# Performance work log

Hardware: AMD Instinct MI355X
Metric: run time of the kernel (lower is better)

Reference implementation:

```python
import jax, jax.numpy as jnp
import numpy as np

AUDIO_DIM, SEM_DIM, ATTN_DIM = 512, 768, 128


def setup_inputs() -> dict:
    key = jax.random.key(0)
    ks = jax.random.split(key, 12)
    B, T, T_sem = 8, 4096, 1024
    s = lambda d: 1.0 / np.sqrt(d)
    return {
        "x_ct": jax.random.normal(ks[0], (B, AUDIO_DIM, T), jnp.float32),
        "sem_btd": jax.random.normal(ks[1], (B, T_sem, SEM_DIM), jnp.float32),
        "ln_w": jnp.ones((AUDIO_DIM,), jnp.float32),
        "ln_b": jnp.zeros((AUDIO_DIM,), jnp.float32),
        "Wq": jax.random.normal(ks[2], (AUDIO_DIM, ATTN_DIM), jnp.float32) * s(AUDIO_DIM),
        "bq": jnp.zeros((ATTN_DIM,), jnp.float32),
        "Wk": jax.random.normal(ks[3], (SEM_DIM, ATTN_DIM), jnp.float32) * s(SEM_DIM),
        "bk": jnp.zeros((ATTN_DIM,), jnp.float32),
        "Wv": jax.random.normal(ks[4], (SEM_DIM, ATTN_DIM), jnp.float32) * s(SEM_DIM),
        "bv": jnp.zeros((ATTN_DIM,), jnp.float32),
        "Wo": jax.random.normal(ks[5], (ATTN_DIM, AUDIO_DIM), jnp.float32) * s(ATTN_DIM),
        "bo": jnp.zeros((AUDIO_DIM,), jnp.float32),
    }


def _layernorm(x, w, b, eps=1e-5):
    mu = jnp.mean(x, axis=-1, keepdims=True)
    var = jnp.mean(jnp.square(x - mu), axis=-1, keepdims=True)
    return (x - mu) * jax.lax.rsqrt(var + eps) * w + b


def reference(x_ct, sem_btd, ln_w, ln_b, Wq, bq, Wk, bk, Wv, bv, Wo, bo):
    # x_ct: [B, C, T] -> [B, T, C]
    x = jnp.swapaxes(x_ct, 1, 2)
    x = _layernorm(x, ln_w, ln_b)
    Q = x @ Wq + bq                      # [B, T, A]
    K = sem_btd @ Wk + bk                # [B, S, A]
    V = sem_btd @ Wv + bv                # [B, S, A]
    scale = ATTN_DIM ** -0.5
    attn = jnp.einsum("bta,bsa->bts", Q, K) * scale
    attn = jax.nn.softmax(attn, axis=-1)  # dropout: eval mode (identity)
    ctx = jnp.einsum("bts,bsa->bta", attn, V)
    delta = ctx @ Wo + bo                # [B, T, C]
    return jnp.swapaxes(delta, 1, 2)     # [B, C, T]
```

## Files before the change

### kernel.cpp

```cpp
#include <hip/hip_runtime.h>
#include <hip/hip_bf16.h>
#include <math.h>

#define BATCH 8
#define TDIM 4096
#define SDIM 1024
#define CDIM 512
#define DDIM 768
#define ADIM 128

typedef short s8v __attribute__((ext_vector_type(8)));
typedef float f4v __attribute__((ext_vector_type(4)));

__device__ __forceinline__ short f2bf(float f) {
    unsigned u = __float_as_uint(f);
    u += 0x7fffu + ((u >> 16) & 1u);
    return (short)(u >> 16);
}
__device__ __forceinline__ float bf2f(short s) {
    return __uint_as_float(((unsigned)(unsigned short)s) << 16);
}
__device__ __forceinline__ f4v mfma16(s8v a, s8v b, f4v c) {
    return __builtin_amdgcn_mfma_f32_16x16x32_bf16(a, b, c, 0, 0, 0);
}
__device__ __forceinline__ void gl_lds16(const short* g, short* l) {
    __builtin_amdgcn_global_load_lds(
        (const __attribute__((address_space(1))) unsigned int*)g,
        (__attribute__((address_space(3))) unsigned int*)l, 16, 0, 0);
}

__global__ __launch_bounds__(256) void prep_w(
    const float* __restrict__ Wq, const float* __restrict__ Wk,
    const float* __restrict__ Wv, const float* __restrict__ Wo,
    const float* __restrict__ lnw,
    short* __restrict__ WqT, short* __restrict__ WkT,
    short* __restrict__ WvT, short* __restrict__ WoT,
    float* __restrict__ uq)
{
    int gid = blockIdx.x * 256 + threadIdx.x;
    if (blockIdx.x == 0) uq[threadIdx.x] = 0.f;
    {
        int k = gid >> 7, n = gid & 127;
        int idx = (k >> 6) * 8192 + n * 64 + ((((k >> 3) & 7) ^ (n & 7)) * 8) + (k & 7);
        WqT[idx] = f2bf(Wq[gid] * lnw[k]);
    }
    #pragma unroll
    for (int i = 0; i < 2; ++i) {
        int e = gid + i * 65536;
        if (e < 98304) {
            int k = e >> 7, n = e & 127;
            WkT[n * 768 + k] = f2bf(Wk[e]);
            WvT[n * 768 + k] = f2bf(Wv[e]);
        }
    }
    {
        int k = gid >> 9, c = gid & 511;
        WoT[c * 128 + k] = f2bf(Wo[gid]);
    }
}

__global__ __launch_bounds__(256) void prep_uv(
    const float* __restrict__ Wq, const float* __restrict__ lnw,
    const float* __restrict__ lnb,
    float* __restrict__ uq, float* __restrict__ vq)
{
    __shared__ float r1[128], r2[128];
    const int a = threadIdx.x & 127, h = threadIdx.x >> 7;
    const int c = blockIdx.x * 2 + h;
    float wv = Wq[c * 128 + a];
    float s1 = bf2f(f2bf(lnw[c] * wv));
    float s2 = lnb[c] * wv;
    if (h) { r1[a] = s1; r2[a] = s2; }
    __syncthreads();
    if (!h) {
        atomicAdd(&uq[a], s1 + r1[a]);
        atomicAdd(&vq[a], s2 + r2[a]);
    }
}

__global__ __launch_bounds__(256) void kv_proj(
    const float* __restrict__ sem,
    const short* __restrict__ WkT, const float* __restrict__ bk,
    const short* __restrict__ WvT, const float* __restrict__ bv,
    short* __restrict__ Kb, short* __restrict__ Vb)
{
    __shared__ __align__(16) short sA[32 * 40];
    __shared__ __align__(16) short sW[2][128 * 40];
    const int tid = threadIdx.x, lane = tid & 63, wave = tid >> 6;
    const int ln15 = lane & 15, q = lane >> 4, kq = q * 8;
    const int r0 = blockIdx.x * 32;
    const int b = r0 >> 10, sbase = r0 & 1023;
    const int kv = wave >> 1;
    const int mh = wave & 1;
    const int m  = mh * 16 + ln15;

    f4v acc[8];
    #pragma unroll
    for (int j = 0; j < 8; ++j) acc[j] = (f4v)0.0f;

    const int srow = tid >> 3;
    const int sk4  = (tid & 7) * 4;

    for (int kc = 0; kc < DDIM / 32; ++kc) {
        __syncthreads();
        {
            float4 f = *(const float4*)&sem[(size_t)(r0 + srow) * DDIM + kc * 32 + sk4];
            uint2 pk;
            pk.x = (unsigned short)f2bf(f.x) | ((unsigned)(unsigned short)f2bf(f.y) << 16);
            pk.y = (unsigned short)f2bf(f.z) | ((unsigned)(unsigned short)f2bf(f.w) << 16);
            *(uint2*)&sA[srow * 40 + sk4] = pk;
        }
        #pragma unroll
        for (int i = 0; i < 2; ++i) {
            int idx8 = i * 256 + tid;
            int n = idx8 >> 2, k8 = (idx8 & 3) * 8;
            *(s8v*)&sW[0][n * 40 + k8] = *(const s8v*)&WkT[(size_t)n * 768 + kc * 32 + k8];
            *(s8v*)&sW[1][n * 40 + k8] = *(const s8v*)&WvT[(size_t)n * 768 + kc * 32 + k8];
        }
        __syncthreads();
        s8v a = *(const s8v*)&sA[m * 40 + kq];
        #pragma unroll
        for (int j = 0; j < 8; ++j) {
            s8v bb = *(const s8v*)&sW[kv][(j * 16 + ln15) * 40 + kq];
            acc[j] = mfma16(a, bb, acc[j]);
        }
    }
    const int s_in_b = sbase + mh * 16 + q * 4;
    if (kv == 0) {
        #pragma unroll
        for (int j = 0; j < 8; ++j) {
            int col = j * 16 + ln15;
            float bias = bk[col];
            #pragma unroll
            for (int r = 0; r < 4; ++r)
                Kb[((size_t)b * SDIM + s_in_b + r) * ADIM + col] = f2bf(acc[j][r] + bias);
        }
    } else {
        #pragma unroll
        for (int j = 0; j < 8; ++j) {
            int col = j * 16 + ln15;
            float bias = bv[col];
            uint2 pk;
            pk.x = (unsigned short)f2bf(acc[j][0] + bias) | ((unsigned)(unsigned short)f2bf(acc[j][1] + bias) << 16);
            pk.y = (unsigned short)f2bf(acc[j][2] + bias) | ((unsigned)(unsigned short)f2bf(acc[j][3] + bias) << 16);
            *(uint2*)&Vb[((size_t)b * ADIM + col) * SDIM + s_in_b] = pk;
        }
    }
}

__global__ __launch_bounds__(512, 4) void ln_q(
    const float* __restrict__ x,
    const short* __restrict__ WqI, const float* __restrict__ uq,
    const float* __restrict__ vq, const float* __restrict__ bq,
    short* __restrict__ Qb)
{
    __shared__ __align__(16) short sX[2][64 * 72];
    __shared__ __align__(16) short sW[2][64 * 128];
    __shared__ __align__(16) float redw[8][16][4][2];
    const int tid = threadIdx.x, lane = tid & 63, wave = tid >> 6;
    const int ln15 = lane & 15, q = lane >> 4, kq = q * 8;
    const int b = blockIdx.x >> 6;
    const int t0 = (blockIdx.x & 63) * 64;
    const float* xb = x + (size_t)b * CDIM * TDIM + t0;

    const int rg = lane >> 4;
    const int g  = rg & 1;
    const int L  = lane & 15;
    const int t4 = L * 4;
    const int crow = wave * 4 + rg;

    float ps1[4] = {0.f,0.f,0.f,0.f}, ps2[4] = {0.f,0.f,0.f,0.f};
    const int wr = wave & 3, wc = wave >> 2;
    const int m = wr * 16 + ln15;
    const int swzm = (m >> 2) & 7;
    f4v acc[4];
    #pragma unroll
    for (int j = 0; j < 4; ++j) acc[j] = (f4v)0.0f;

    float4 xv[2];

#define PROC_X(BUF) do {                                                      \
    _Pragma("unroll")                                                         \
    for (int i = 0; i < 2; ++i) {                                             \
        float4 v = xv[i];                                                     \
        ps1[0] += v.x; ps2[0] += v.x * v.x;                                   \
        ps1[1] += v.y; ps2[1] += v.y * v.y;                                   \
        ps1[2] += v.z; ps2[2] += v.z * v.z;                                   \
        ps1[3] += v.w; ps2[3] += v.w * v.w;                                   \
        float o0 = __shfl_xor(v.x, 16); float o1 = __shfl_xor(v.y, 16);       \
        float o2 = __shfl_xor(v.z, 16); float o3 = __shfl_xor(v.w, 16);       \
        const int c   = crow + i * 32;                                        \
        const int cdw = c & ~1;                                               \
        unsigned wA, wB; int tA, tB;                                          \
        if (g == 0) {                                                         \
            tA = t4; tB = t4 + 1;                                             \
            wA = (unsigned short)f2bf(v.x) | ((unsigned)(unsigned short)f2bf(o0) << 16); \
            wB = (unsigned short)f2bf(v.y) | ((unsigned)(unsigned short)f2bf(o1) << 16); \
        } else {                                                              \
            tA = t4 + 2; tB = t4 + 3;                                         \
            wA = (unsigned short)f2bf(o2) | ((unsigned)(unsigned short)f2bf(v.z) << 16); \
            wB = (unsigned short)f2bf(o3) | ((unsigned)(unsigned short)f2bf(v.w) << 16); \
        }                                                                     \
        *(unsigned*)&sX[BUF][tA * 72 + (((cdw >> 3) ^ ((tA >> 2) & 7)) * 8) + (cdw & 7)] = wA; \
        *(unsigned*)&sX[BUF][tB * 72 + (((cdw >> 3) ^ ((tB >> 2) & 7)) * 8) + (cdw & 7)] = wB; \
    }                                                                         \
} while (0)

    xv[0] = *(const float4*)&xb[(size_t)crow * TDIM + t4];
    xv[1] = *(const float4*)&xb[(size_t)(crow + 32) * TDIM + t4];
    #pragma unroll
    for (int i = 0; i < 2; ++i) {
        int gi = i * 512 + wave * 64;
        gl_lds16(&WqI[(size_t)(gi + lane) * 8], &sW[0][gi * 8]);
    }
    PROC_X(0);
    __syncthreads();

    for (int kc = 0; kc < 8; ++kc) {
        const int cur = kc & 1;
        if (kc < 7) {
            const float* xc = xb + (size_t)(kc + 1) * 64 * TDIM;
            xv[0] = *(const float4*)&xc[(size_t)crow * TDIM + t4];
            xv[1] = *(const float4*)&xc[(size_t)(crow + 32) * TDIM + t4];
            const short* wch = WqI + (size_t)(kc + 1) * 8192;
            #pragma unroll
            for (int i = 0; i < 2; ++i) {
                int gi = i * 512 + wave * 64;
                gl_lds16(&wch[(size_t)(gi + lane) * 8], &sW[cur ^ 1][gi * 8]);
            }
        }
        #pragma unroll
        for (int kk = 0; kk < 2; ++kk) {
            s8v a = *(const s8v*)&sX[cur][m * 72 + (((kk * 4 + q) ^ swzm) * 8)];
            #pragma unroll
            for (int j = 0; j < 4; ++j) {
                int n = wc * 64 + j * 16 + ln15;
                s8v bb = *(const s8v*)&sW[cur][n * 64 + (((kk * 4 + q) ^ (n & 7)) * 8)];
                acc[j] = mfma16(a, bb, acc[j]);
            }
        }
        if (kc < 7) PROC_X(cur ^ 1);
        __syncthreads();
    }

    #pragma unroll
    for (int mk = 16; mk <= 32; mk <<= 1) {
        #pragma unroll
        for (int jj = 0; jj < 4; ++jj) {
            ps1[jj] += __shfl_xor(ps1[jj], mk);
            ps2[jj] += __shfl_xor(ps2[jj], mk);
        }
    }
    if (lane < 16) {
        #pragma unroll
        for (int jj = 0; jj < 4; ++jj) {
            redw[wave][L][jj][0] = ps1[jj];
            redw[wave][L][jj][1] = ps2[jj];
        }
    }
    __syncthreads();

    float u4[4], v4[4];
    #pragma unroll
    for (int j = 0; j < 4; ++j) {
        int col = wc * 64 + j * 16 + ln15;
        u4[j] = uq[col]; v4[j] = vq[col] + bq[col];
    }
    const float scale = 0.08838834764831845f;
    const int quad = wr * 4 + q;
    #pragma unroll
    for (int r = 0; r < 4; ++r) {
        float s1 = 0.f, s2 = 0.f;
        #pragma unroll
        for (int w = 0; w < 8; ++w) {
            float2 p = *(const float2*)&redw[w][quad][r][0];
            s1 += p.x; s2 += p.y;
        }
        float mu = s1 * (1.f / 512.f);
        float var = s2 * (1.f / 512.f) - mu * mu;
        float rs = rsqrtf(var + 1e-5f);
        int t = t0 + wr * 16 + q * 4 + r;
        #pragma unroll
        for (int j = 0; j < 4; ++j) {
            float qv = (rs * (acc[j][r] - mu * u4[j]) + v4[j]) * scale;
            Qb[((size_t)b * TDIM + t) * ADIM + (wc * 64 + j * 16 + ln15)] = f2bf(qv);
        }
    }
#undef PROC_X
}

__global__ __launch_bounds__(256) void attn(
    const short* __restrict__ Qb, const short* __restrict__ Kb,
    const short* __restrict__ Vb, short* __restrict__ Cx)
{
    __shared__ __align__(16) short sK [2][64 * 128];
    __shared__ __align__(16) short sVT[2][128 * 64];
    __shared__ __align__(16) short sP [64 * 64];
    const int tid = threadIdx.x, lane = tid & 63, wave = tid >> 6;
    const int ln15 = lane & 15, q = lane >> 4, kq = q * 8;
    const int b = blockIdx.x >> 6;
    const int t0 = (blockIdx.x & 63) * 64;
    const int m = wave * 16 + ln15;

    const int krow = tid >> 4, kkb = tid & 15;
    const int varow = tid >> 3, vkb = tid & 7;

    s8v qf[4];
    {
        const short* qp = Qb + ((size_t)b * TDIM + t0 + m) * ADIM + kq;
        #pragma unroll
        for (int kc = 0; kc < 4; ++kc) qf[kc] = *(const s8v*)(qp + kc * 32);
    }
    s8v ones;
    #pragma unroll
    for (int j = 0; j < 8; ++j) ones[j] = (short)0x3F80;

    f4v accO[8]; f4v accL = (f4v)0.0f;
    #pragma unroll
    for (int j = 0; j < 8; ++j) accO[j] = (f4v)0.0f;

    const short* Kbase = Kb + (size_t)b * SDIM * ADIM;
    const short* Vbase = Vb + (size_t)b * ADIM * SDIM;
    s8v rk[4], rv[4];

    #pragma unroll
    for (int i = 0; i < 4; ++i) {
        rk[i] = *(const s8v*)(Kbase + (size_t)(i * 16 + krow) * ADIM + kkb * 8);
        rv[i] = *(const s8v*)(Vbase + (size_t)(i * 32 + varow) * SDIM + vkb * 8);
    }
    #pragma unroll
    for (int i = 0; i < 4; ++i) {
        int r = i * 16 + krow;
        *(s8v*)&sK[0][r * 128 + ((kkb ^ (r & 15)) * 8)] = rk[i];
        int a = i * 32 + varow;
        *(s8v*)&sVT[0][a * 64 + ((vkb ^ (a & 7)) * 8)] = rv[i];
    }
    __syncthreads();

    for (int sc = 0; sc < SDIM / 64; ++sc) {
        const int cur = sc & 1;
        if (sc < 15) {
            const int s0n = (sc + 1) * 64;
            #pragma unroll
            for (int i = 0; i < 4; ++i) {
                rk[i] = *(const s8v*)(Kbase + (size_t)(s0n + i * 16 + krow) * ADIM + kkb * 8);
                rv[i] = *(const s8v*)(Vbase + (size_t)(i * 32 + varow) * SDIM + s0n + vkb * 8);
            }
        }
        #pragma unroll
        for (int j = 0; j < 4; ++j) {
            f4v sacc = (f4v)0.0f;
            const int row = j * 16 + ln15;
            #pragma unroll
            for (int kc = 0; kc < 4; ++kc) {
                s8v bb = *(const s8v*)&sK[cur][row * 128 + (((kc * 4 + q) ^ (row & 15)) * 8)];
                sacc = mfma16(qf[kc], bb, sacc);
            }
            #pragma unroll
            for (int r = 0; r < 4; ++r) {
                float ev = __expf(sacc[r]);
                int prow = wave * 16 + q * 4 + r;
                int pcol = j * 16 + ln15;
                sP[prow * 64 + (((pcol >> 3) ^ (prow & 7)) * 8) + (pcol & 7)] = f2bf(ev);
            }
        }
        #pragma unroll
        for (int kc = 0; kc < 2; ++kc) {
            s8v pa = *(const s8v*)&sP[m * 64 + (((kc * 4 + q) ^ (m & 7)) * 8)];
            accL = mfma16(pa, ones, accL);
            #pragma unroll
            for (int j = 0; j < 8; ++j) {
                int a = j * 16 + ln15;
                s8v bb = *(const s8v*)&sVT[cur][a * 64 + (((kc * 4 + q) ^ (a & 7)) * 8)];
                accO[j] = mfma16(pa, bb, accO[j]);
            }
        }
        if (sc < 15) {
            #pragma unroll
            for (int i = 0; i < 4; ++i) {
                int r = i * 16 + krow;
                *(s8v*)&sK[cur ^ 1][r * 128 + ((kkb ^ (r & 15)) * 8)] = rk[i];
                int a = i * 32 + varow;
                *(s8v*)&sVT[cur ^ 1][a * 64 + ((vkb ^ (a & 7)) * 8)] = rv[i];
            }
        }
        __syncthreads();
    }
    #pragma unroll
    for (int r = 0; r < 4; ++r) {
        float rinv = 1.0f / accL[r];
        int t = t0 + wave * 16 + q * 4 + r;
        #pragma unroll
        for (int j = 0; j < 8; ++j) {
            int col = j * 16 + ln15;
            Cx[((size_t)b * TDIM + t) * ADIM + col] = f2bf(accO[j][r] * rinv);
        }
    }
}

__global__ __launch_bounds__(256) void out_proj(
    const short* __restrict__ Cx, const short* __restrict__ WoT,
    const float* __restrict__ bo, float* __restrict__ out)
{
    __shared__ __align__(16) short sCtx[64 * 136];
    __shared__ __align__(16) char  buf[128 * 136 * 2];
    short* sWoT = (short*)buf;
    float* outT = (float*)buf;
    const int tid = threadIdx.x, lane = tid & 63, wave = tid >> 6;
    const int ln15 = lane & 15, q = lane >> 4, kq = q * 8;
    const int b = blockIdx.x >> 8;
    const int rem = blockIdx.x & 255;
    const int t0 = (rem & 63) * 64;
    const int c0 = (rem >> 6) * 128;

    #pragma unroll
    for (int i = 0; i < 4; ++i) {
        int idx8 = i * 256 + tid;
        int row = idx8 >> 4, a8 = (idx8 & 15) * 8;
        *(s8v*)&sCtx[row * 136 + a8] = *(const s8v*)&Cx[((size_t)b * TDIM + t0 + row) * ADIM + a8];
    }
    #pragma unroll
    for (int i = 0; i < 8; ++i) {
        int idx8 = i * 256 + tid;
        int n = idx8 >> 4, k8 = (idx8 & 15) * 8;
        *(s8v*)&sWoT[n * 136 + k8] = *(const s8v*)&WoT[(size_t)(c0 + n) * ADIM + k8];
    }
    __syncthreads();
    f4v acc[8];
    #pragma unroll
    for (int j = 0; j < 8; ++j) acc[j] = (f4v)0.0f;
    const int m = wave * 16 + ln15;
    #pragma unroll
    for (int kc = 0; kc < 4; ++kc) {
        s8v a = *(const s8v*)&sCtx[m * 136 + kc * 32 + kq];
        #pragma unroll
        for (int j = 0; j < 8; ++j) {
            s8v bb = *(const s8v*)&sWoT[(j * 16 + ln15) * 136 + kc * 32 + kq];
            acc[j] = mfma16(a, bb, acc[j]);
        }
    }
    __syncthreads();
    #pragma unroll
    for (int j = 0; j < 8; ++j) {
        int cl = j * 16 + ln15;
        float bias = bo[c0 + cl];
        #pragma unroll
        for (int r = 0; r < 4; ++r) {
            int tl = wave * 16 + q * 4 + r;
            outT[cl * 68 + tl] = acc[j][r] + bias;
        }
    }
    __syncthreads();
    #pragma unroll
    for (int i = 0; i < 8; ++i) {
        int idx4 = i * 256 + tid;
        int c = idx4 >> 4, t4 = (idx4 & 15) * 4;
        float4 v = *(const float4*)&outT[c * 68 + t4];
        *(float4*)&out[((size_t)b * CDIM + c0 + c) * TDIM + t0 + t4] = v;
    }
}

extern "C" void kernel_launch(void* const* d_in, const int* in_sizes, int n_in,
                              void* d_out, int out_size, void* d_ws, size_t ws_size,
                              hipStream_t stream) {
    const float* x   = (const float*)d_in[0];
    const float* sem = (const float*)d_in[1];
    const float* lnw = (const float*)d_in[2];
    const float* lnb = (const float*)d_in[3];
    const float* Wq  = (const float*)d_in[4];
    const float* bq  = (const float*)d_in[5];
    const float* Wk  = (const float*)d_in[6];
    const float* bk  = (const float*)d_in[7];
    const float* Wv  = (const float*)d_in[8];
    const float* bv  = (const float*)d_in[9];
    const float* Wo  = (const float*)d_in[10];
    const float* bo  = (const float*)d_in[11];
    float* out = (float*)d_out;

    short* ws  = (short*)d_ws;
    short* Qb  = ws;
    short* Kb  = Qb  + (size_t)BATCH * TDIM * ADIM;
    short* Vb  = Kb  + (size_t)BATCH * SDIM * ADIM;
    short* Cx  = Vb  + (size_t)BATCH * SDIM * ADIM;
    short* WqT = Cx  + (size_t)BATCH * TDIM * ADIM;
    short* WkT = WqT + 128 * 512;
    short* WvT = WkT + 128 * 768;
    short* WoT = WvT + 128 * 768;
    float* uq  = (float*)(WoT + 512 * 128);
    float* vq  = uq + 128;

    hipLaunchKernelGGL(prep_w,  dim3(256),  dim3(256), 0, stream,
                       Wq, Wk, Wv, Wo, lnw, WqT, WkT, WvT, WoT, uq);
    hipLaunchKernelGGL(prep_uv, dim3(256),  dim3(256), 0, stream, Wq, lnw, lnb, uq, vq);
    hipLaunchKernelGGL(kv_proj, dim3(256),  dim3(256), 0, stream, sem, WkT, bk, WvT, bv, Kb, Vb);
    hipLaunchKernelGGL(ln_q,    dim3(512),  dim3(512), 0, stream, x, WqT, uq, vq, bq, Qb);
    hipLaunchKernelGGL(attn,    dim3(512),  dim3(256), 0, stream, Qb, Kb, Vb, Cx);
    hipLaunchKernelGGL(out_proj,dim3(2048), dim3(256), 0, stream, Cx, WoT, bo, out);
}
```

Baseline: 234.1 us.

## Merge prep kernels and co-schedule LN-Q with KV projection in one launch

After: 232.9 us. Within noise of the previous version (-0.5%).

```diff
diff --git a/kernel.cpp b/kernel.cpp
--- a/kernel.cpp
+++ b/kernel.cpp
@@ -29,155 +29,88 @@
         (__attribute__((address_space(3))) unsigned int*)l, 16, 0, 0);
 }
 
-__global__ __launch_bounds__(256) void prep_w(
+__global__ __launch_bounds__(256) void prep(
     const float* __restrict__ Wq, const float* __restrict__ Wk,
     const float* __restrict__ Wv, const float* __restrict__ Wo,
-    const float* __restrict__ lnw,
+    const float* __restrict__ lnw, const float* __restrict__ lnb,
     short* __restrict__ WqT, short* __restrict__ WkT,
     short* __restrict__ WvT, short* __restrict__ WoT,
-    float* __restrict__ uq)
-{
-    int gid = blockIdx.x * 256 + threadIdx.x;
-    if (blockIdx.x == 0) uq[threadIdx.x] = 0.f;
-    {
-        int k = gid >> 7, n = gid & 127;
-        int idx = (k >> 6) * 8192 + n * 64 + ((((k >> 3) & 7) ^ (n & 7)) * 8) + (k & 7);
-        WqT[idx] = f2bf(Wq[gid] * lnw[k]);
-    }
-    #pragma unroll
-    for (int i = 0; i < 2; ++i) {
-        int e = gid + i * 65536;
-        if (e < 98304) {
-            int k = e >> 7, n = e & 127;
-            WkT[n * 768 + k] = f2bf(Wk[e]);
-            WvT[n * 768 + k] = f2bf(Wv[e]);
-        }
-    }
-    {
-        int k = gid >> 9, c = gid & 511;
-        WoT[c * 128 + k] = f2bf(Wo[gid]);
-    }
-}
-
-__global__ __launch_bounds__(256) void prep_uv(
-    const float* __restrict__ Wq, const float* __restrict__ lnw,
-    const float* __restrict__ lnb,
     float* __restrict__ uq, float* __restrict__ vq)
 {
     __shared__ float r1[128], r2[128];
-    const int a = threadIdx.x & 127, h = threadIdx.x >> 7;
-    const int c = blockIdx.x * 2 + h;
-    float wv = Wq[c * 128 + a];
-    float s1 = bf2f(f2bf(lnw[c] * wv));
-    float s2 = lnb[c] * wv;
-    if (h) { r1[a] = s1; r2[a] = s2; }
-    __syncthreads();
-    if (!h) {
-        atomicAdd(&uq[a], s1 + r1[a]);
-        atomicAdd(&vq[a], s2 + r2[a]);
-    }
-}
-
-__global__ __launch_bounds__(256) void kv_proj(
+    if (blockIdx.x < 256) {
+        int gid = blockIdx.x * 256 + threadIdx.x;
+        {
+            int k = gid >> 7, n = gid & 127;
+            int idx = (k >> 6) * 8192 + n * 64 + ((((k >> 3) & 7) ^ (n & 7)) * 8) + (k & 7);
+            WqT[idx] = f2bf(Wq[gid] * lnw[k]);
+        }
+        #pragma unroll
+        for (int i = 0; i < 2; ++i) {
+            int e = gid + i * 65536;
+            if (e < 98304) {
+                int k = e >> 7, n = e & 127;
+                WkT[n * 768 + k] = f2bf(Wk[e]);
+                WvT[n * 768 + k] = f2bf(Wv[e]);
+            }
+        }
+        {
+            int k = gid >> 9, c = gid & 511;
+            WoT[c * 128 + k] = f2bf(Wo[gid]);
+        }
+    } else {
+        const int a = threadIdx.x & 127, h = threadIdx.x >> 7;
+        const int c = (blockIdx.x - 256) * 2 + h;
+        float wv = Wq[c * 128 + a];
+        float s1 = bf2f(f2bf(lnw[c] * wv));
+        float s2 = lnb[c] * wv;
+        if (h) { r1[a] = s1; r2[a] = s2; }
+        __syncthreads();
+        if (!h) {
+            atomicAdd(&uq[a], s1 + r1[a]);
+            atomicAdd(&vq[a], s2 + r2[a]);
+        }
+    }
+}
+
+__global__ __launch_bounds__(512, 4) void mid(
+    const float* __restrict__ x, const short* __restrict__ WqI,
+    const float* __restrict__ uq, const float* __restrict__ vq,
+    const float* __restrict__ bq, short* __restrict__ Qb,
     const float* __restrict__ sem,
     const short* __restrict__ WkT, const float* __restrict__ bk,
     const short* __restrict__ WvT, const float* __restrict__ bv,
     short* __restrict__ Kb, short* __restrict__ Vb)
 {
-    __shared__ __align__(16) short sA[32 * 40];
-    __shared__ __align__(16) short sW[2][128 * 40];
+    __shared__ __align__(16) char smem[55296];
     const int tid = threadIdx.x, lane = tid & 63, wave = tid >> 6;
     const int ln15 = lane & 15, q = lane >> 4, kq = q * 8;
-    const int r0 = blockIdx.x * 32;
-    const int b = r0 >> 10, sbase = r0 & 1023;
-    const int kv = wave >> 1;
-    const int mh = wave & 1;
-    const int m  = mh * 16 + ln15;
-
-    f4v acc[8];
-    #pragma unroll
-    for (int j = 0; j < 8; ++j) acc[j] = (f4v)0.0f;
-
-    const int srow = tid >> 3;
-    const int sk4  = (tid & 7) * 4;
-
-    for (int kc = 0; kc < DDIM / 32; ++kc) {
-        __syncthreads();
-        {
-            float4 f = *(const float4*)&sem[(size_t)(r0 + srow) * DDIM + kc * 32 + sk4];
-            uint2 pk;
-            pk.x = (unsigned short)f2bf(f.x) | ((unsigned)(unsigned short)f2bf(f.y) << 16);
-            pk.y = (unsigned short)f2bf(f.z) | ((unsigned)(unsigned short)f2bf(f.w) << 16);
-            *(uint2*)&sA[srow * 40 + sk4] = pk;
-        }
-        #pragma unroll
-        for (int i = 0; i < 2; ++i) {
-            int idx8 = i * 256 + tid;
-            int n = idx8 >> 2, k8 = (idx8 & 3) * 8;
-            *(s8v*)&sW[0][n * 40 + k8] = *(const s8v*)&WkT[(size_t)n * 768 + kc * 32 + k8];
-            *(s8v*)&sW[1][n * 40 + k8] = *(const s8v*)&WvT[(size_t)n * 768 + kc * 32 + k8];
-        }
-        __syncthreads();
-        s8v a = *(const s8v*)&sA[m * 40 + kq];
-        #pragma unroll
-        for (int j = 0; j < 8; ++j) {
-            s8v bb = *(const s8v*)&sW[kv][(j * 16 + ln15) * 40 + kq];
-            acc[j] = mfma16(a, bb, acc[j]);
-        }
-    }
-    const int s_in_b = sbase + mh * 16 + q * 4;
-    if (kv == 0) {
-        #pragma unroll
-        for (int j = 0; j < 8; ++j) {
-            int col = j * 16 + ln15;
-            float bias = bk[col];
-            #pragma unroll
-            for (int r = 0; r < 4; ++r)
-                Kb[((size_t)b * SDIM + s_in_b + r) * ADIM + col] = f2bf(acc[j][r] + bias);
-        }
-    } else {
-        #pragma unroll
-        for (int j = 0; j < 8; ++j) {
-            int col = j * 16 + ln15;
-            float bias = bv[col];
-            uint2 pk;
-            pk.x = (unsigned short)f2bf(acc[j][0] + bias) | ((unsigned)(unsigned short)f2bf(acc[j][1] + bias) << 16);
-            pk.y = (unsigned short)f2bf(acc[j][2] + bias) | ((unsigned)(unsigned short)f2bf(acc[j][3] + bias) << 16);
-            *(uint2*)&Vb[((size_t)b * ADIM + col) * SDIM + s_in_b] = pk;
-        }
-    }
-}
-
-__global__ __launch_bounds__(512, 4) void ln_q(
-    const float* __restrict__ x,
-    const short* __restrict__ WqI, const float* __restrict__ uq,
-    const float* __restrict__ vq, const float* __restrict__ bq,
-    short* __restrict__ Qb)
-{
-    __shared__ __align__(16) short sX[2][64 * 72];
-    __shared__ __align__(16) short sW[2][64 * 128];
-    __shared__ __align__(16) float redw[8][16][4][2];
-    const int tid = threadIdx.x, lane = tid & 63, wave = tid >> 6;
-    const int ln15 = lane & 15, q = lane >> 4, kq = q * 8;
-    const int b = blockIdx.x >> 6;
-    const int t0 = (blockIdx.x & 63) * 64;
-    const float* xb = x + (size_t)b * CDIM * TDIM + t0;
-
-    const int rg = lane >> 4;
-    const int g  = rg & 1;
-    const int L  = lane & 15;
-    const int t4 = L * 4;
-    const int crow = wave * 4 + rg;
-
-    float ps1[4] = {0.f,0.f,0.f,0.f}, ps2[4] = {0.f,0.f,0.f,0.f};
-    const int wr = wave & 3, wc = wave >> 2;
-    const int m = wr * 16 + ln15;
-    const int swzm = (m >> 2) & 7;
-    f4v acc[4];
-    #pragma unroll
-    for (int j = 0; j < 4; ++j) acc[j] = (f4v)0.0f;
-
-    float4 xv[2];
+    const int bid = blockIdx.x;
+
+    if ((bid % 3) != 2) {
+        const int ln_id = (bid / 3) * 2 + (bid % 3);
+        short* sXp = (short*)smem;
+        short* sWp = (short*)(smem + 18432);
+        float* redwp = (float*)(smem + 51200);
+        const int b = ln_id >> 6;
+        const int t0 = (ln_id & 63) * 64;
+        const float* xb = x + (size_t)b * CDIM * TDIM + t0;
+
+        const int rg = lane >> 4;
+        const int g  = rg & 1;
+        const int L  = lane & 15;
+        const int t4 = L * 4;
+        const int crow = wave * 4 + rg;
+
+        float ps1[4] = {0.f,0.f,0.f,0.f}, ps2[4] = {0.f,0.f,0.f,0.f};
+        const int wr = wave & 3, wc = wave >> 2;
+        const int m = wr * 16 + ln15;
+        const int swzm = (m >> 2) & 7;
+        f4v acc[4];
+        #pragma unroll
+        for (int j = 0; j < 4; ++j) acc[j] = (f4v)0.0f;
+
+        float4 xv[2];
 
 #define PROC_X(BUF) do {                                                      \
     _Pragma("unroll")                                                         \
@@ -201,92 +134,159 @@
             wA = (unsigned short)f2bf(o2) | ((unsigned)(unsigned short)f2bf(v.z) << 16); \
             wB = (unsigned short)f2bf(o3) | ((unsigned)(unsigned short)f2bf(v.w) << 16); \
         }                                                                     \
-        *(unsigned*)&sX[BUF][tA * 72 + (((cdw >> 3) ^ ((tA >> 2) & 7)) * 8) + (cdw & 7)] = wA; \
-        *(unsigned*)&sX[BUF][tB * 72 + (((cdw >> 3) ^ ((tB >> 2) & 7)) * 8) + (cdw & 7)] = wB; \
+        *(unsigned*)&sXp[(BUF) * 4608 + tA * 72 + (((cdw >> 3) ^ ((tA >> 2) & 7)) * 8) + (cdw & 7)] = wA; \
+        *(unsigned*)&sXp[(BUF) * 4608 + tB * 72 + (((cdw >> 3) ^ ((tB >> 2) & 7)) * 8) + (cdw & 7)] = wB; \
     }                                                                         \
 } while (0)
 
-    xv[0] = *(const float4*)&xb[(size_t)crow * TDIM + t4];
-    xv[1] = *(const float4*)&xb[(size_t)(crow + 32) * TDIM + t4];
-    #pragma unroll
-    for (int i = 0; i < 2; ++i) {
-        int gi = i * 512 + wave * 64;
-        gl_lds16(&WqI[(size_t)(gi + lane) * 8], &sW[0][gi * 8]);
-    }
-    PROC_X(0);
-    __syncthreads();
-
-    for (int kc = 0; kc < 8; ++kc) {
-        const int cur = kc & 1;
-        if (kc < 7) {
-            const float* xc = xb + (size_t)(kc + 1) * 64 * TDIM;
-            xv[0] = *(const float4*)&xc[(size_t)crow * TDIM + t4];
-            xv[1] = *(const float4*)&xc[(size_t)(crow + 32) * TDIM + t4];
-            const short* wch = WqI + (size_t)(kc + 1) * 8192;
-            #pragma unroll
-            for (int i = 0; i < 2; ++i) {
-                int gi = i * 512 + wave * 64;
-                gl_lds16(&wch[(size_t)(gi + lane) * 8], &sW[cur ^ 1][gi * 8]);
-            }
-        }
-        #pragma unroll
-        for (int kk = 0; kk < 2; ++kk) {
-            s8v a = *(const s8v*)&sX[cur][m * 72 + (((kk * 4 + q) ^ swzm) * 8)];
+        xv[0] = *(const float4*)&xb[(size_t)crow * TDIM + t4];
+        xv[1] = *(const float4*)&xb[(size_t)(crow + 32) * TDIM + t4];
+        #pragma unroll
+        for (int i = 0; i < 2; ++i) {
+            int gi = i * 512 + wave * 64;
+            gl_lds16(&WqI[(size_t)(gi + lane) * 8], &sWp[gi * 8]);
+        }
+        PROC_X(0);
+        __syncthreads();
+
+        for (int kc = 0; kc < 8; ++kc) {
+            const int cur = kc & 1;
+            if (kc < 7) {
+                const float* xc = xb + (size_t)(kc + 1) * 64 * TDIM;
+                xv[0] = *(const float4*)&xc[(size_t)crow * TDIM + t4];
+                xv[1] = *(const float4*)&xc[(size_t)(crow + 32) * TDIM + t4];
+                const short* wch = WqI + (size_t)(kc + 1) * 8192;
+                #pragma unroll
+                for (int i = 0; i < 2; ++i) {
+                    int gi = i * 512 + wave * 64;
+                    gl_lds16(&wch[(size_t)(gi + lane) * 8], &sWp[(cur ^ 1) * 8192 + gi * 8]);
+                }
+            }
+            #pragma unroll
+            for (int kk = 0; kk < 2; ++kk) {
+                s8v a = *(const s8v*)&sXp[cur * 4608 + m * 72 + (((kk * 4 + q) ^ swzm) * 8)];
+                #pragma unroll
+                for (int j = 0; j < 4; ++j) {
+                    int n = wc * 64 + j * 16 + ln15;
+                    s8v bb = *(const s8v*)&sWp[cur * 8192 + n * 64 + (((kk * 4 + q) ^ (n & 7)) * 8)];
+                    acc[j] = mfma16(a, bb, acc[j]);
+                }
+            }
+            if (kc < 7) PROC_X(cur ^ 1);
+            __syncthreads();
+        }
+#undef PROC_X
+
+        #pragma unroll
+        for (int mk = 16; mk <= 32; mk <<= 1) {
+            #pragma unroll
+            for (int jj = 0; jj < 4; ++jj) {
+                ps1[jj] += __shfl_xor(ps1[jj], mk);
+                ps2[jj] += __shfl_xor(ps2[jj], mk);
+            }
+        }
+        if (lane < 16) {
+            #pragma unroll
+            for (int jj = 0; jj < 4; ++jj) {
+                redwp[((wave * 16 + L) * 4 + jj) * 2 + 0] = ps1[jj];
+                redwp[((wave * 16 + L) * 4 + jj) * 2 + 1] = ps2[jj];
+            }
+        }
+        __syncthreads();
+
+        float u4[4], v4[4];
+        #pragma unroll
+        for (int j = 0; j < 4; ++j) {
+            int col = wc * 64 + j * 16 + ln15;
+            u4[j] = uq[col]; v4[j] = vq[col] + bq[col];
+        }
+        const float scale = 0.08838834764831845f;
+        const int quad = wr * 4 + q;
+        #pragma unroll
+        for (int r = 0; r < 4; ++r) {
+            float s1 = 0.f, s2 = 0.f;
+            #pragma unroll
+            for (int w = 0; w < 8; ++w) {
+                float2 p = *(const float2*)&redwp[((w * 16 + quad) * 4 + r) * 2];
+                s1 += p.x; s2 += p.y;
+            }
+            float mu = s1 * (1.f / 512.f);
+            float var = s2 * (1.f / 512.f) - mu * mu;
+            float rs = rsqrtf(var + 1e-5f);
+            int t = t0 + wr * 16 + q * 4 + r;
             #pragma unroll
             for (int j = 0; j < 4; ++j) {
-                int n = wc * 64 + j * 16 + ln15;
-                s8v bb = *(const s8v*)&sW[cur][n * 64 + (((kk * 4 + q) ^ (n & 7)) * 8)];
-                acc[j] = mfma16(a, bb, acc[j]);
-            }
-        }
-        if (kc < 7) PROC_X(cur ^ 1);
-        __syncthreads();
-    }
-
-    #pragma unroll
-    for (int mk = 16; mk <= 32; mk <<= 1) {
-        #pragma unroll
-        for (int jj = 0; jj < 4; ++jj) {
-            ps1[jj] += __shfl_xor(ps1[jj], mk);
-            ps2[jj] += __shfl_xor(ps2[jj], mk);
-        }
-    }
-    if (lane < 16) {
-        #pragma unroll
-        for (int jj = 0; jj < 4; ++jj) {
-            redw[wave][L][jj][0] = ps1[jj];
-            redw[wave][L][jj][1] = ps2[jj];
-        }
-    }
-    __syncthreads();
-
-    float u4[4], v4[4];
-    #pragma unroll
-    for (int j = 0; j < 4; ++j) {
-        int col = wc * 64 + j * 16 + ln15;
-        u4[j] = uq[col]; v4[j] = vq[col] + bq[col];
-    }
-    const float scale = 0.08838834764831845f;
-    const int quad = wr * 4 + q;
-    #pragma unroll
-    for (int r = 0; r < 4; ++r) {
-        float s1 = 0.f, s2 = 0.f;
-        #pragma unroll
-        for (int w = 0; w < 8; ++w) {
-            float2 p = *(const float2*)&redw[w][quad][r][0];
-            s1 += p.x; s2 += p.y;
-        }
-        float mu = s1 * (1.f / 512.f);
-        float var = s2 * (1.f / 512.f) - mu * mu;
-        float rs = rsqrtf(var + 1e-5f);
-        int t = t0 + wr * 16 + q * 4 + r;
-        #pragma unroll
-        for (int j = 0; j < 4; ++j) {
-            float qv = (rs * (acc[j][r] - mu * u4[j]) + v4[j]) * scale;
-            Qb[((size_t)b * TDIM + t) * ADIM + (wc * 64 + j * 16 + ln15)] = f2bf(qv);
-        }
-    }
-#undef PROC_X
+                float qv = (rs * (acc[j][r] - mu * u4[j]) + v4[j]) * scale;
+                Qb[((size_t)b * TDIM + t) * ADIM + (wc * 64 + j * 16 + ln15)] = f2bf(qv);
+            }
+        }
+    } else {
+        const int kv_id = bid / 3;
+        if (tid < 256) {
+            short* sA  = (short*)smem;
+            short* sWk = (short*)(smem + 2560);
+            const int r0 = kv_id * 32;
+            const int b = r0 >> 10, sbase = r0 & 1023;
+            const int kv = wave >> 1;
+            const int mh = wave & 1;
+            const int m  = mh * 16 + ln15;
+
+            f4v acc[8];
+            #pragma unroll
+            for (int j = 0; j < 8; ++j) acc[j] = (f4v)0.0f;
+
+            const int srow = tid >> 3;
+            const int sk4  = (tid & 7) * 4;
+
+            for (int kc = 0; kc < DDIM / 32; ++kc) {
+                __syncthreads();
+                {
+                    float4 f = *(const float4*)&sem[(size_t)(r0 + srow) * DDIM + kc * 32 + sk4];
+                    uint2 pk;
+                    pk.x = (unsigned short)f2bf(f.x) | ((unsigned)(unsigned short)f2bf(f.y) << 16);
+                    pk.y = (unsigned short)f2bf(f.z) | ((unsigned)(unsigned short)f2bf(f.w) << 16);
+                    *(uint2*)&sA[srow * 40 + sk4] = pk;
+                }
+                #pragma unroll
+                for (int i = 0; i < 2; ++i) {
+                    int idx8 = i * 256 + tid;
+                    int n = idx8 >> 2, k8 = (idx8 & 3) * 8;
+                    *(s8v*)&sWk[n * 40 + k8] = *(const s8v*)&WkT[(size_t)n * 768 + kc * 32 + k8];
+                    *(s8v*)&sWk[5120 + n * 40 + k8] = *(const s8v*)&WvT[(size_t)n * 768 + kc * 32 + k8];
+                }
+                __syncthreads();
+                s8v a = *(const s8v*)&sA[m * 40 + kq];
+                #pragma unroll
+                for (int j = 0; j < 8; ++j) {
+                    s8v bb = *(const s8v*)&sWk[kv * 5120 + (j * 16 + ln15) * 40 + kq];
+                    acc[j] = mfma16(a, bb, acc[j]);
+                }
+            }
+            const int s_in_b = sbase + mh * 16 + q * 4;
+            if (kv == 0) {
+                #pragma unroll
+                for (int j = 0; j < 8; ++j) {
+                    int col = j * 16 + ln15;
+                    float bias = bk[col];
+                    #pragma unroll
+                    for (int r = 0; r < 4; ++r)
+                        Kb[((size_t)b * SDIM + s_in_b + r) * ADIM + col] = f2bf(acc[j][r] + bias);
+                }
+            } else {
+                #pragma unroll
+                for (int j = 0; j < 8; ++j) {
+                    int col = j * 16 + ln15;
+                    float bias = bv[col];
+                    uint2 pk;
+                    pk.x = (unsigned short)f2bf(acc[j][0] + bias) | ((unsigned)(unsigned short)f2bf(acc[j][1] + bias) << 16);
+                    pk.y = (unsigned short)f2bf(acc[j][2] + bias) | ((unsigned)(unsigned short)f2bf(acc[j][3] + bias) << 16);
+                    *(uint2*)&Vb[((size_t)b * ADIM + col) * SDIM + s_in_b] = pk;
+                }
+            }
+        } else {
+            for (int kc = 0; kc < DDIM / 32; ++kc) { __syncthreads(); __syncthreads(); }
+        }
+    }
 }
 
 __global__ __launch_bounds__(256) void attn(
@@ -489,11 +489,11 @@
     float* uq  = (float*)(WoT + 512 * 128);
     float* vq  = uq + 128;
 
-    hipLaunchKernelGGL(prep_w,  dim3(256),  dim3(256), 0, stream,
-                       Wq, Wk, Wv, Wo, lnw, WqT, WkT, WvT, WoT, uq);
-    hipLaunchKernelGGL(prep_uv, dim3(256),  dim3(256), 0, stream, Wq, lnw, lnb, uq, vq);
-    hipLaunchKernelGGL(kv_proj, dim3(256),  dim3(256), 0, stream, sem, WkT, bk, WvT, bv, Kb, Vb);
-    hipLaunchKernelGGL(ln_q,    dim3(512),  dim3(512), 0, stream, x, WqT, uq, vq, bq, Qb);
-    hipLaunchKernelGGL(attn,    dim3(512),  dim3(256), 0, stream, Qb, Kb, Vb, Cx);
-    hipLaunchKernelGGL(out_proj,dim3(2048), dim3(256), 0, stream, Cx, WoT, bo, out);
-}
+    hipMemsetAsync(uq, 0, 256 * sizeof(float), stream);
+    hipLaunchKernelGGL(prep, dim3(512), dim3(256), 0, stream,
+                       Wq, Wk, Wv, Wo, lnw, lnb, WqT, WkT, WvT, WoT, uq, vq);
+    hipLaunchKernelGGL(mid,  dim3(768), dim3(512), 0, stream,
+                       x, WqT, uq, vq, bq, Qb, sem, WkT, bk, WvT, bv, Kb, Vb);
+    hipLaunchKernelGGL(attn, dim3(512), dim3(256), 0, stream, Qb, Kb, Vb, Cx);
+    hipLaunchKernelGGL(out_proj, dim3(2048), dim3(256), 0, stream, Cx, WoT, bo, out);
+}
```
